# Kernel optimization log

Measured on AMD Instinct MI355X. Metric: run time of the kernel, lower is better.

## Reference

```python
import jax, jax.numpy as jnp
import numpy as np

N_NODES = 50000
N_EDGES = 1600000
N_FEAT = 128
DROPOUT = 0.1


def setup_inputs() -> dict:
    key = jax.random.key(0)
    k1, k2, k3, k4 = jax.random.split(key, 4)
    x = jax.random.normal(k1, (N_NODES, N_FEAT), dtype=jnp.float32)
    adj_vals = jax.random.uniform(k2, (N_EDGES,), dtype=jnp.float32)
    row = jax.random.randint(k3, (N_EDGES,), 0, N_NODES, dtype=jnp.int32)
    col = jax.random.randint(k4, (N_EDGES,), 0, N_NODES, dtype=jnp.int32)
    return {"x": x, "adj_vals": adj_vals, "row": row, "col": col}


def reference(x, adj_vals, row, col):
    # MixedDropout on sparse adjacency values (deterministic fixed key),
    # then SpMM: out[i] = sum_{e: row[e]==i} A_drop[e] * x[col[e]]
    keep_prob = 1.0 - DROPOUT
    mask_key = jax.random.fold_in(jax.random.key(42), 7)
    keep = jax.random.bernoulli(mask_key, keep_prob, adj_vals.shape)
    vals_drop = jnp.where(keep, adj_vals / keep_prob, 0.0)
    # gather source features and weight by (dropped) edge values
    msgs = vals_drop[:, None] * x[col]  # [E, F]
    out = jax.ops.segment_sum(msgs, row, num_segments=N_NODES)  # [N, F]
    return out
```

## Files before the change

kernel.cpp:

```cpp
#include <hip/hip_runtime.h>
#include <stdint.h>

#define N_NODES 50000
#define N_EDGES 1600000
#define N_FEAT 128
#define CAP 64
#define OVF_CAP 65536

#define RSHIFT 8
#define BROWS 256
#define NB 196
#define NWG_A 256
#define A_THREADS 1024
#define CAPW 56
#define EPW (N_EDGES / NWG_A)


struct KeyPair { uint32_t a, b; };

__host__ __device__ constexpr inline uint32_t rotl32(uint32_t x, int r) {
  return (x << r) | (x >> (32 - r));
}

__host__ __device__ constexpr inline KeyPair threefry2x32(uint32_t k0, uint32_t k1,
                                                          uint32_t x0, uint32_t x1) {
  const uint32_t ks0 = k0, ks1 = k1, ks2 = k0 ^ k1 ^ 0x1BD11BDAu;
  x0 += ks0;
  x1 += ks1;
  const int rotA[4] = {13, 15, 26, 6};
  const int rotB[4] = {17, 29, 16, 24};
  const uint32_t ks[3] = {ks0, ks1, ks2};
  for (int i = 0; i < 5; ++i) {
    const int* rot = (i & 1) ? rotB : rotA;
    for (int j = 0; j < 4; ++j) {
      x0 += x1;
      x1 = rotl32(x1, rot[j]);
      x1 ^= x0;
    }
    x0 += ks[(i + 1) % 3];
    x1 += ks[(i + 2) % 3] + (uint32_t)(i + 1);
  }
  return {x0, x1};
}

constexpr KeyPair MASK_KEY = threefry2x32(0u, 42u, 0u, 7u);

__device__ inline bool edge_keep(uint32_t e) {
  KeyPair r = threefry2x32(MASK_KEY.a, MASK_KEY.b, 0u, e);
  uint32_t bits = r.a ^ r.b;
  float u = __uint_as_float((bits >> 9) | 0x3f800000u) - 1.0f;
  return u < 0.9f;
}

__device__ inline uint32_t f2bf(uint32_t b) {
  return (b + 0x7fffu + ((b >> 16) & 1u)) >> 16;
}


__global__ void __launch_bounds__(A_THREADS) convA_kernel(const float* __restrict__ x,
                                                          uint32_t* __restrict__ xb,
                                                          const float* __restrict__ adj_vals,
                                                          const int* __restrict__ row,
                                                          const int* __restrict__ col,
                                                          uint64_t* __restrict__ coarse,
                                                          uint32_t* __restrict__ lens,
                                                          uint32_t* __restrict__ ovf_count,
                                                          uint64_t* __restrict__ ovf) {
  __shared__ uint32_t cnt[NB];
  int wg = blockIdx.x;
  int tid = threadIdx.x;
  if (tid < NB) cnt[tid] = 0;

  const int gthreads = NWG_A * A_THREADS;
  for (int i = wg * A_THREADS + tid; i < (N_NODES * N_FEAT) / 4; i += gthreads) {
    float4 f = ((const float4*)x)[i];
    uint2 o;
    o.x = f2bf(__float_as_uint(f.x)) | (f2bf(__float_as_uint(f.y)) << 16);
    o.y = f2bf(__float_as_uint(f.z)) | (f2bf(__float_as_uint(f.w)) << 16);
    ((uint2*)xb)[i] = o;
  }
  __syncthreads();

  int e0 = wg * EPW;
  int e1 = e0 + EPW;
  for (int e = e0 + tid; e < e1; e += A_THREADS) {
    if (!edge_keep((uint32_t)e)) continue;
    float v = adj_vals[e] / 0.9f;
    uint32_t r = (uint32_t)row[e];
    uint32_t c = (uint32_t)col[e];
    uint32_t b = r >> RSHIFT;
    uint32_t li = atomicAdd(&cnt[b], 1u);
    uint64_t p = ((uint64_t)r << 48) | ((uint64_t)c << 32) | (uint64_t)__float_as_uint(v);
    if (li < CAPW) {
      coarse[((size_t)b * NWG_A + wg) * CAPW + li] = p;
    } else {
      uint32_t oi = atomicAdd(ovf_count, 1u);
      if (oi < OVF_CAP) ovf[oi] = p;
    }
  }
  __syncthreads();
  if (tid < NB) lens[(size_t)tid * NWG_A + wg] = min(cnt[tid], (uint32_t)CAPW);
}

__global__ void __launch_bounds__(1024) partB_kernel(const uint64_t* __restrict__ coarse,
                                                     const uint32_t* __restrict__ lens,
                                                     uint32_t* __restrict__ payload,
                                                     uint32_t* __restrict__ cursor,
                                                     uint32_t* __restrict__ ovf_count,
                                                     uint64_t* __restrict__ ovf) {
  int b = blockIdx.x;
  int tid = threadIdx.x;
  __shared__ uint32_t s[NWG_A];
  __shared__ uint32_t cnt[BROWS];
  if (tid < NWG_A) s[tid] = lens[(size_t)b * NWG_A + tid];
  if (tid < BROWS) cnt[tid] = 0;
  __syncthreads();
  for (int off = 1; off < NWG_A; off <<= 1) {
    uint32_t v = 0, u = 0;
    if (tid < NWG_A) {
      v = s[tid];
      u = (tid >= off) ? s[tid - off] : 0u;
    }
    __syncthreads();
    if (tid < NWG_A) s[tid] = v + u;
    __syncthreads();
  }
  int seg = tid >> 2;
  int sub = tid & 3;
  uint32_t sbase = (seg == 0) ? 0u : s[seg - 1];
  uint32_t slen = s[seg] - sbase;
  const uint64_t* cseg = coarse + ((size_t)b * NWG_A + seg) * CAPW;
  for (uint32_t li = (uint32_t)sub; li < slen; li += 4) {
    uint64_t p = cseg[li];
    uint32_t r = (uint32_t)(p >> 48);
    uint32_t rl = r & (BROWS - 1);
    uint32_t idx = atomicAdd(&cnt[rl], 1u);
    if (idx < CAP) {
      uint32_t c = (uint32_t)(p >> 32) & 0xFFFFu;
      payload[(size_t)r * CAP + idx] = (c << 16) | f2bf((uint32_t)p);
    } else {
      uint32_t oi = atomicAdd(ovf_count, 1u);
      if (oi < OVF_CAP) ovf[oi] = p;
    }
  }
  __syncthreads();
  for (int k = tid; k < BROWS; k += 1024) {
    uint32_t r = ((uint32_t)b << RSHIFT) + (uint32_t)k;
    if (r < N_NODES) {
      uint32_t c0 = min(cnt[k], (uint32_t)CAP);
      cursor[r] = r * CAP + c0;
      uint32_t np = min((c0 + 7u) & ~7u, (uint32_t)CAP);
      for (uint32_t i2 = c0; i2 < np; ++i2) payload[(size_t)r * CAP + i2] = 0u;
    }
  }
}

__global__ void __launch_bounds__(256) gather_bf16_kernel(const uint32_t* __restrict__ xb,
                                                          const uint32_t* __restrict__ payload,
                                                          const uint32_t* __restrict__ cursor,
                                                          float* __restrict__ out) {
  int r = blockIdx.x * 8 + (threadIdx.x >> 5);
  int lane = threadIdx.x & 31;
  uint32_t base = (uint32_t)r * CAP;
  uint32_t cnt = cursor[r] - base;
  uint32_t n = (cnt + 7u) & ~7u;
  const uint2* x2 = (const uint2*)xb;
  float4 acc = make_float4(0.f, 0.f, 0.f, 0.f);

  uint32_t p = payload[base + lane];

#define GSTEP(ww)                                                            \
  {                                                                          \
    uint32_t cc = (ww) >> 16;                                                \
    float vv = __uint_as_float((ww) << 16);                                  \
    uint2 a = x2[(size_t)cc * 32 + lane];                                    \
    float f0 = __uint_as_float(a.x << 16);                                   \
    float f1 = __uint_as_float(a.x & 0xffff0000u);                           \
    float f2 = __uint_as_float(a.y << 16);                                   \
    float f3 = __uint_as_float(a.y & 0xffff0000u);                           \
    acc.x += vv * f0; acc.y += vv * f1;                                      \
    acc.z += vv * f2; acc.w += vv * f3;                                      \
  }

  int n0 = (int)min(n, 32u);
  for (int j = 0; j < n0; j += 8) {
    uint32_t w0 = __shfl(p, j + 0, 32);
    uint32_t w1 = __shfl(p, j + 1, 32);
    uint32_t w2 = __shfl(p, j + 2, 32);
    uint32_t w3 = __shfl(p, j + 3, 32);
    uint32_t w4 = __shfl(p, j + 4, 32);
    uint32_t w5 = __shfl(p, j + 5, 32);
    uint32_t w6 = __shfl(p, j + 6, 32);
    uint32_t w7 = __shfl(p, j + 7, 32);
    GSTEP(w0) GSTEP(w1) GSTEP(w2) GSTEP(w3)
    GSTEP(w4) GSTEP(w5) GSTEP(w6) GSTEP(w7)
  }
  if (n > 32) {
    uint32_t q = payload[base + 32 + lane];
    int n1 = (int)(n - 32u);
    for (int j = 0; j < n1; j += 8) {
      uint32_t w0 = __shfl(q, j + 0, 32);
      uint32_t w1 = __shfl(q, j + 1, 32);
      uint32_t w2 = __shfl(q, j + 2, 32);
      uint32_t w3 = __shfl(q, j + 3, 32);
      uint32_t w4 = __shfl(q, j + 4, 32);
      uint32_t w5 = __shfl(q, j + 5, 32);
      uint32_t w6 = __shfl(q, j + 6, 32);
      uint32_t w7 = __shfl(q, j + 7, 32);
      GSTEP(w0) GSTEP(w1) GSTEP(w2) GSTEP(w3)
      GSTEP(w4) GSTEP(w5) GSTEP(w6) GSTEP(w7)
    }
  }
#undef GSTEP
  ((float4*)out)[(size_t)r * 32 + lane] = acc;
}

__global__ void __launch_bounds__(256) ovf_pack_kernel(const float* __restrict__ x,
                                                       const uint32_t* __restrict__ ovf_count,
                                                       const uint64_t* __restrict__ ovf,
                                                       float* __restrict__ out) {
  uint32_t n = *ovf_count;
  if (n > OVF_CAP) n = OVF_CAP;
  int g = (int)((blockIdx.x * blockDim.x + threadIdx.x) >> 7);
  int f = threadIdx.x & 127;
  const int ngroups = (64 * 256) >> 7;
  for (uint32_t oi = g; oi < n; oi += ngroups) {
    uint64_t p = ovf[oi];
    uint32_t r = (uint32_t)(p >> 48);
    uint32_t c = (uint32_t)((p >> 32) & 0xFFFFu);
    float v = __uint_as_float((uint32_t)p);
    atomicAdd(&out[(size_t)r * N_FEAT + f], v * x[(size_t)c * N_FEAT + f]);
  }
}


__global__ void __launch_bounds__(256) scatter_fused_kernel(const float* __restrict__ x,
                                                            const float* __restrict__ adj_vals,
                                                            const int* __restrict__ row,
                                                            const int* __restrict__ col,
                                                            float* __restrict__ out) {
  long long t = (long long)blockIdx.x * blockDim.x + threadIdx.x;
  int e = (int)(t >> 6);
  int lane = (int)(t & 63);
  if (e >= N_EDGES) return;
  if (!edge_keep((uint32_t)e)) return;
  float v = adj_vals[e] / 0.9f;
  float2 xf = *(const float2*)(x + (long long)col[e] * N_FEAT + lane * 2);
  float* dst = out + (long long)row[e] * N_FEAT + lane * 2;
  atomicAdd(dst, v * xf.x);
  atomicAdd(dst + 1, v * xf.y);
}


extern "C" void kernel_launch(void* const* d_in, const int* in_sizes, int n_in,
                              void* d_out, int out_size, void* d_ws, size_t ws_size,
                              hipStream_t stream) {
  const float* x        = (const float*)d_in[0];
  const float* adj_vals = (const float*)d_in[1];
  const int*   row      = (const int*)d_in[2];
  const int*   col      = (const int*)d_in[3];
  float* out = (float*)d_out;

  size_t a_cursor  = 0;
  size_t a_ovfc    = (a_cursor + (size_t)N_NODES * 4 + 255) & ~255ull;
  size_t a_ovf     = (a_ovfc + 4 + 255) & ~255ull;
  size_t a_lens    = (a_ovf + (size_t)OVF_CAP * 8 + 255) & ~255ull;
  size_t a_coarse  = (a_lens + (size_t)NB * NWG_A * 4 + 255) & ~255ull;
  size_t a_payload = (a_coarse + (size_t)NB * NWG_A * CAPW * 8 + 255) & ~255ull;
  size_t a_xb      = (a_payload + (size_t)N_NODES * CAP * 4 + 255) & ~255ull;
  size_t need      = a_xb + (size_t)N_NODES * N_FEAT * 2;

  if (ws_size >= need) {
    uint32_t* cursor    = (uint32_t*)((char*)d_ws + a_cursor);
    uint32_t* ovf_count = (uint32_t*)((char*)d_ws + a_ovfc);
    uint64_t* ovf       = (uint64_t*)((char*)d_ws + a_ovf);
    uint32_t* lens      = (uint32_t*)((char*)d_ws + a_lens);
    uint64_t* coarse    = (uint64_t*)((char*)d_ws + a_coarse);
    uint32_t* payload   = (uint32_t*)((char*)d_ws + a_payload);
    uint32_t* xb        = (uint32_t*)((char*)d_ws + a_xb);

    hipMemsetAsync(ovf_count, 0, 4, stream);
    convA_kernel<<<NWG_A, A_THREADS, 0, stream>>>(x, xb, adj_vals, row, col,
                                                  coarse, lens, ovf_count, ovf);
    partB_kernel<<<NB, 1024, 0, stream>>>(coarse, lens, payload, cursor, ovf_count, ovf);
    gather_bf16_kernel<<<N_NODES / 8, 256, 0, stream>>>(xb, payload, cursor, out);
    ovf_pack_kernel<<<64, 256, 0, stream>>>(x, ovf_count, ovf, out);
  } else {
    hipMemsetAsync(d_out, 0, (size_t)out_size * sizeof(float), stream);
    long long total_threads = (long long)N_EDGES * 64;
    scatter_fused_kernel<<<(int)((total_threads + 255) / 256), 256, 0, stream>>>(
        x, adj_vals, row, col, out);
  }
}
```

Measured before the change: 169.1 us.

## Replace fixed-capacity coarse buckets with counted, prefix-scanned per-workgroup bucket layout

The first kernel now makes two passes over its edge slice: one counts kept edges per row-block, then a shared-memory scan gives bucket offsets, and a second pass writes packed edges contiguously into a per-workgroup region. This drops the fixed per-bucket capacity and its global overflow path, and removes the scan from the second kernel, which now reads precomputed lengths and segment bases. The cost is recomputing the dropout hash and rereading row for every edge, plus scattered per-bucket reads in the second kernel. The gather macro is also reformatted without changing what it computes.

```diff
diff --git a/kernel.cpp b/kernel.cpp
--- a/kernel.cpp
+++ b/kernel.cpp
@@ -12,8 +12,8 @@
 #define NB 196
 #define NWG_A 256
 #define A_THREADS 1024
-#define CAPW 56
 #define EPW (N_EDGES / NWG_A)
+#define CSTRIDE 6272
 
 
 struct KeyPair { uint32_t a, b; };
@@ -64,12 +64,14 @@
                                                           const int* __restrict__ col,
                                                           uint64_t* __restrict__ coarse,
                                                           uint32_t* __restrict__ lens,
-                                                          uint32_t* __restrict__ ovf_count,
-                                                          uint64_t* __restrict__ ovf) {
+                                                          uint32_t* __restrict__ segbase) {
   __shared__ uint32_t cnt[NB];
+  __shared__ uint32_t base[NB];
+  __shared__ uint32_t fill[NB];
+  __shared__ uint32_t s[NB];
   int wg = blockIdx.x;
   int tid = threadIdx.x;
-  if (tid < NB) cnt[tid] = 0;
+  if (tid < NB) { cnt[tid] = 0; fill[tid] = 0; }
 
   const int gthreads = NWG_A * A_THREADS;
   for (int i = wg * A_THREADS + tid; i < (N_NODES * N_FEAT) / 4; i += gthreads) {
@@ -85,51 +87,58 @@
   int e1 = e0 + EPW;
   for (int e = e0 + tid; e < e1; e += A_THREADS) {
     if (!edge_keep((uint32_t)e)) continue;
+    atomicAdd(&cnt[(uint32_t)row[e] >> RSHIFT], 1u);
+  }
+  __syncthreads();
+
+  if (tid < NB) s[tid] = cnt[tid];
+  __syncthreads();
+  for (int off = 1; off < 256; off <<= 1) {
+    uint32_t v = 0, u = 0;
+    if (tid < NB) {
+      v = s[tid];
+      u = (tid >= off) ? s[tid - off] : 0u;
+    }
+    __syncthreads();
+    if (tid < NB) s[tid] = v + u;
+    __syncthreads();
+  }
+  if (tid < NB) {
+    uint32_t bb = s[tid] - cnt[tid];
+    base[tid] = bb;
+    lens[(size_t)tid * NWG_A + wg] = cnt[tid];
+    segbase[(size_t)tid * NWG_A + wg] = bb;
+  }
+  __syncthreads();
+
+  uint64_t* my = coarse + (size_t)wg * CSTRIDE;
+  for (int e = e0 + tid; e < e1; e += A_THREADS) {
+    if (!edge_keep((uint32_t)e)) continue;
     float v = adj_vals[e] / 0.9f;
     uint32_t r = (uint32_t)row[e];
     uint32_t c = (uint32_t)col[e];
     uint32_t b = r >> RSHIFT;
-    uint32_t li = atomicAdd(&cnt[b], 1u);
-    uint64_t p = ((uint64_t)r << 48) | ((uint64_t)c << 32) | (uint64_t)__float_as_uint(v);
-    if (li < CAPW) {
-      coarse[((size_t)b * NWG_A + wg) * CAPW + li] = p;
-    } else {
-      uint32_t oi = atomicAdd(ovf_count, 1u);
-      if (oi < OVF_CAP) ovf[oi] = p;
-    }
-  }
-  __syncthreads();
-  if (tid < NB) lens[(size_t)tid * NWG_A + wg] = min(cnt[tid], (uint32_t)CAPW);
+    uint32_t pos = base[b] + atomicAdd(&fill[b], 1u);
+    my[pos] = ((uint64_t)r << 48) | ((uint64_t)c << 32) | (uint64_t)__float_as_uint(v);
+  }
 }
 
 __global__ void __launch_bounds__(1024) partB_kernel(const uint64_t* __restrict__ coarse,
                                                      const uint32_t* __restrict__ lens,
+                                                     const uint32_t* __restrict__ segbase,
                                                      uint32_t* __restrict__ payload,
                                                      uint32_t* __restrict__ cursor,
                                                      uint32_t* __restrict__ ovf_count,
                                                      uint64_t* __restrict__ ovf) {
+  __shared__ uint32_t cnt[BROWS];
   int b = blockIdx.x;
   int tid = threadIdx.x;
-  __shared__ uint32_t s[NWG_A];
-  __shared__ uint32_t cnt[BROWS];
-  if (tid < NWG_A) s[tid] = lens[(size_t)b * NWG_A + tid];
   if (tid < BROWS) cnt[tid] = 0;
   __syncthreads();
-  for (int off = 1; off < NWG_A; off <<= 1) {
-    uint32_t v = 0, u = 0;
-    if (tid < NWG_A) {
-      v = s[tid];
-      u = (tid >= off) ? s[tid - off] : 0u;
-    }
-    __syncthreads();
-    if (tid < NWG_A) s[tid] = v + u;
-    __syncthreads();
-  }
   int seg = tid >> 2;
   int sub = tid & 3;
-  uint32_t sbase = (seg == 0) ? 0u : s[seg - 1];
-  uint32_t slen = s[seg] - sbase;
-  const uint64_t* cseg = coarse + ((size_t)b * NWG_A + seg) * CAPW;
+  uint32_t slen = lens[(size_t)b * NWG_A + seg];
+  const uint64_t* cseg = coarse + (size_t)seg * CSTRIDE + segbase[(size_t)b * NWG_A + seg];
   for (uint32_t li = (uint32_t)sub; li < slen; li += 4) {
     uint64_t p = cseg[li];
     uint32_t r = (uint32_t)(p >> 48);
@@ -174,12 +183,10 @@
     uint32_t cc = (ww) >> 16;                                                \
     float vv = __uint_as_float((ww) << 16);                                  \
     uint2 a = x2[(size_t)cc * 32 + lane];                                    \
-    float f0 = __uint_as_float(a.x << 16);                                   \
-    float f1 = __uint_as_float(a.x & 0xffff0000u);                           \
-    float f2 = __uint_as_float(a.y << 16);                                   \
-    float f3 = __uint_as_float(a.y & 0xffff0000u);                           \
-    acc.x += vv * f0; acc.y += vv * f1;                                      \
-    acc.z += vv * f2; acc.w += vv * f3;                                      \
+    acc.x += vv * __uint_as_float(a.x << 16);                                \
+    acc.y += vv * __uint_as_float(a.x & 0xffff0000u);                        \
+    acc.z += vv * __uint_as_float(a.y << 16);                                \
+    acc.w += vv * __uint_as_float(a.y & 0xffff0000u);                        \
   }
 
   int n0 = (int)min(n, 32u);
@@ -261,28 +268,31 @@
   const int*   col      = (const int*)d_in[3];
   float* out = (float*)d_out;
 
-  size_t a_cursor  = 0;
-  size_t a_ovfc    = (a_cursor + (size_t)N_NODES * 4 + 255) & ~255ull;
+  size_t a_ovfc    = 0;
   size_t a_ovf     = (a_ovfc + 4 + 255) & ~255ull;
   size_t a_lens    = (a_ovf + (size_t)OVF_CAP * 8 + 255) & ~255ull;
-  size_t a_coarse  = (a_lens + (size_t)NB * NWG_A * 4 + 255) & ~255ull;
-  size_t a_payload = (a_coarse + (size_t)NB * NWG_A * CAPW * 8 + 255) & ~255ull;
+  size_t a_segb    = (a_lens + (size_t)NB * NWG_A * 4 + 255) & ~255ull;
+  size_t a_cursor  = (a_segb + (size_t)NB * NWG_A * 4 + 255) & ~255ull;
+  size_t a_coarse  = (a_cursor + (size_t)N_NODES * 4 + 255) & ~255ull;
+  size_t a_payload = (a_coarse + (size_t)NWG_A * CSTRIDE * 8 + 255) & ~255ull;
   size_t a_xb      = (a_payload + (size_t)N_NODES * CAP * 4 + 255) & ~255ull;
   size_t need      = a_xb + (size_t)N_NODES * N_FEAT * 2;
 
   if (ws_size >= need) {
-    uint32_t* cursor    = (uint32_t*)((char*)d_ws + a_cursor);
     uint32_t* ovf_count = (uint32_t*)((char*)d_ws + a_ovfc);
     uint64_t* ovf       = (uint64_t*)((char*)d_ws + a_ovf);
     uint32_t* lens      = (uint32_t*)((char*)d_ws + a_lens);
+    uint32_t* segbase   = (uint32_t*)((char*)d_ws + a_segb);
+    uint32_t* cursor    = (uint32_t*)((char*)d_ws + a_cursor);
     uint64_t* coarse    = (uint64_t*)((char*)d_ws + a_coarse);
     uint32_t* payload   = (uint32_t*)((char*)d_ws + a_payload);
     uint32_t* xb        = (uint32_t*)((char*)d_ws + a_xb);
 
     hipMemsetAsync(ovf_count, 0, 4, stream);
     convA_kernel<<<NWG_A, A_THREADS, 0, stream>>>(x, xb, adj_vals, row, col,
-                                                  coarse, lens, ovf_count, ovf);
-    partB_kernel<<<NB, 1024, 0, stream>>>(coarse, lens, payload, cursor, ovf_count, ovf);
+                                                  coarse, lens, segbase);
+    partB_kernel<<<NB, 1024, 0, stream>>>(coarse, lens, segbase, payload, cursor,
+                                          ovf_count, ovf);
     gather_bf16_kernel<<<N_NODES / 8, 256, 0, stream>>>(xb, payload, cursor, out);
     ovf_pack_kernel<<<64, 256, 0, stream>>>(x, ovf_count, ovf, out);
   } else {
```

Result: no change. 169.8 us (+0.4%).
